# Kernel tuning notes

Hardware: AMD Instinct MI355X
Metric: run time of the kernel (lower is better)

Reference implementation:

```python
import jax, jax.numpy as jnp
import numpy as np

TIME_SCALES = [1, 2, 4]
K = len(TIME_SCALES)      # 3 scales
N = 4                     # lcm(time_scales)
S = sum(TIME_SCALES)      # 7 slots
D_HEAD = 128              # d
D = S * D_HEAD            # 896
IO_DIM = 1024
RANK = 64
HIDDEN = 4 * D            # 3584
EPS = 1e-5


def _tables():
    active = np.empty((N, K), dtype=np.int64)
    perm = np.empty((N, K, N), dtype=np.int64)
    inv = np.empty((N, K, N), dtype=np.int64)
    ids = np.arange(N)
    for ph in range(N):
        off = 0
        for k, s in enumerate(TIME_SCALES):
            active[ph, k] = off + ph % s
            off += s
            j = ph % s
            alpha = N // s
            p = (ids + alpha * j) % N   # SHARED assignment
            perm[ph, k] = p
            ip = np.empty_like(p)
            ip[p] = ids
            inv[ph, k] = ip
    return active, perm, inv

ACTIVE, PERM, INV = _tables()


def _ln(x, scale, bias):
    mu = jnp.mean(x, axis=-1, keepdims=True)
    var = jnp.mean((x - mu) ** 2, axis=-1, keepdims=True)
    return (x - mu) * jax.lax.rsqrt(var + EPS) * scale + bias


def setup_inputs() -> dict:
    key = jax.random.key(0)
    ks = jax.random.split(key, 16)
    B, T = 8, 1024

    def w(k, shape, s=0.02):
        return jax.random.normal(k, shape, dtype=jnp.float32) * s

    return {
        "x": jax.random.normal(ks[0], (B, T, IO_DIM), dtype=jnp.float32),
        "enc_base_w": w(ks[1], (D, IO_DIM)),
        "enc_A_w": w(ks[2], (RANK, IO_DIM)),
        "enc_B": w(ks[3], (RANK, N, D)),
        "enc_beta": jnp.float32(0.01),
        "Wqkv": w(ks[4], (K, N, D_HEAD, 3 * D_HEAD)),
        "ln_attn_scale": jnp.ones((D_HEAD,), jnp.float32),
        "ln_attn_bias": jnp.zeros((D_HEAD,), jnp.float32),
        "ln_mixer_scale": jnp.ones((D,), jnp.float32),
        "ln_mixer_bias": jnp.zeros((D,), jnp.float32),
        "mixer_w1": w(ks[5], (HIDDEN, D)),
        "mixer_b1": jnp.zeros((HIDDEN,), jnp.float32),
        "mixer_w2": w(ks[6], (D, HIDDEN)),
        "mixer_b2": jnp.zeros((D,), jnp.float32),
        "dec_ln_scale": jnp.ones((N * D,), jnp.float32),
        "dec_ln_bias": jnp.zeros((N * D,), jnp.float32),
        "dec_down_w": w(ks[7], (RANK, N * D)),
        "dec_up_w": w(ks[8], (IO_DIM, RANK)),
        "phase": 1,
    }


def reference(x, enc_base_w, enc_A_w, enc_B, enc_beta, Wqkv,
              ln_attn_scale, ln_attn_bias, ln_mixer_scale, ln_mixer_bias,
              mixer_w1, mixer_b1, mixer_w2, mixer_b2,
              dec_ln_scale, dec_ln_bias, dec_down_w, dec_up_w, phase):
    B, T, _ = x.shape
    # ---- StreamLoRAEncoder: x [B,T,io] -> z0 [B,T,N,D]
    base = x @ enc_base_w.T                 # [B,T,D]
    h = x @ enc_A_w.T                       # [B,T,r]
    delta = jnp.einsum('btr,rnd->btnd', h, enc_B)
    z0 = base[:, :, None, :] + enc_beta * delta
    # ---- gather active slots for this phase (one slot per scale group)
    slots = ACTIVE[phase]                   # [K]
    z_slots = z0.reshape(B, T, N, S, D_HEAD)
    x_slot = z_slots[:, :, :, slots, :]     # [B,T,N,K,d]
    x_slot = _ln(x_slot, ln_attn_scale, ln_attn_bias)
    # ---- SHARED qkv projection (stream->head inverse perm, bmm, head->stream perm)
    x_in = x_slot.transpose(0, 1, 3, 2, 4)  # [B,T,K,N,d]
    kk = np.arange(K)[:, None]
    x_head = x_in[:, :, kk, INV[phase], :]  # [B,T,K,N,d]
    qkv = jnp.einsum('btknd,knde->btkne', x_head, Wqkv)  # [B,T,K,N,3d]
    qh, kh, vh = jnp.split(qkv, 3, axis=-1)
    p = PERM[phase]
    q = qh[:, :, kk, p, :].transpose(0, 3, 2, 1, 4).reshape(B, N * K, T, D_HEAD)
    k_ = kh[:, :, kk, p, :].transpose(0, 3, 2, 1, 4).reshape(B, N * K, T, D_HEAD)
    v = vh[:, :, kk, p, :].transpose(0, 3, 2, 1, 4).reshape(B, N * K, T, D_HEAD)
    # ---- causal attention over T per (stream, scale) head
    scores = jnp.einsum('bhtd,bhsd->bhts', q, k_) / np.float32(np.sqrt(D_HEAD))
    mask = jnp.tril(jnp.ones((T, T), dtype=bool))
    scores = jnp.where(mask, scores, jnp.float32(-1e9))
    attn = jax.nn.softmax(scores, axis=-1)
    out = jnp.einsum('bhts,bhsd->bhtd', attn, v)  # [B,N*K,T,d]
    # ---- scatter back to active slots (residual add)
    out5 = out.reshape(B, N, K, T, D_HEAD).transpose(0, 3, 1, 2, 4)  # [B,T,N,K,d]
    z1 = z_slots.at[:, :, :, slots, :].add(out5).reshape(B, T, N, D)
    # ---- mixer MLP (pre-LN residual)
    hm = _ln(z1, ln_mixer_scale, ln_mixer_bias)
    m = jax.nn.gelu(hm @ mixer_w1.T + mixer_b1, approximate=False) @ mixer_w2.T + mixer_b2
    z2 = z1 + m
    # ---- StreamLoRADecoder: concat streams, LN, rank-bottleneck projection
    cat = z2.reshape(B, T, N * D)
    y = _ln(cat, dec_ln_scale, dec_ln_bias) @ dec_down_w.T @ dec_up_w.T
    return y
```

## Files before the change

kernel.cpp:

```cpp
#include <hip/hip_runtime.h>
#include <hip/hip_bf16.h>
#include <math.h>


#define BT   8192
#define DH   128
#define DD   896
#define ND   3584
#define IO   1024
#define RK   64
#define HID  3584

typedef __attribute__((ext_vector_type(8))) short short8;
typedef __attribute__((ext_vector_type(4))) float f32x4;
typedef __hip_bfloat16 bf16;

__device__ __forceinline__ float gelu_f(float v)
{
    float u = v * 0.70710678118654752f;
    float a = fabsf(u);
    float t = __builtin_amdgcn_rcpf(1.0f + 0.3275911f * a);
    float p = t * (0.254829592f + t * (-0.284496736f + t * (1.421413741f +
              t * (-1.453152027f + t * 1.061405429f))));
    float er = 1.0f - p * __expf(-u * u);
    er = copysignf(er, u);
    return 0.5f * v * (1.0f + er);
}

template<int BM, int BN, int BK, int TM, int TN>
__global__ __launch_bounds__(256) void gemm_kernel(const float* __restrict__ A,
                                                   const float* __restrict__ B,
                                                   float* __restrict__ C,
                                                   int N, int Kd)
{
    constexpr int THREADS = (BM / TM) * (BN / TN);
    constexpr int LDA = BM + 4;
    constexpr int LDB = BN + 4;
    __shared__ float As[BK][LDA];
    __shared__ float Bs[BK][LDB];

    const int tid = threadIdx.x;
    constexpr int NX = BN / TN;
    const int tx = tid % NX;
    const int ty = tid / NX;
    const int row0 = blockIdx.y * BM;
    const int col0 = blockIdx.x * BN;

    float acc[TM][TN];
#pragma unroll
    for (int i = 0; i < TM; ++i)
#pragma unroll
        for (int j = 0; j < TN; ++j) acc[i][j] = 0.f;

    for (int k0 = 0; k0 < Kd; k0 += BK) {
        constexpr int AF4 = BM * BK / 4;
        for (int f = tid; f < AF4; f += THREADS) {
            int r  = f / (BK / 4);
            int c4 = (f % (BK / 4)) * 4;
            float4 v = *(const float4*)(A + (size_t)(row0 + r) * Kd + k0 + c4);
            As[c4 + 0][r] = v.x; As[c4 + 1][r] = v.y;
            As[c4 + 2][r] = v.z; As[c4 + 3][r] = v.w;
        }
        constexpr int BF4 = BN * BK / 4;
        for (int f = tid; f < BF4; f += THREADS) {
            int r  = f / (BK / 4);
            int c4 = (f % (BK / 4)) * 4;
            float4 v = *(const float4*)(B + (size_t)(col0 + r) * Kd + k0 + c4);
            Bs[c4 + 0][r] = v.x; Bs[c4 + 1][r] = v.y;
            Bs[c4 + 2][r] = v.z; Bs[c4 + 3][r] = v.w;
        }
        __syncthreads();

#pragma unroll
        for (int kk = 0; kk < BK; ++kk) {
            float a[TM], b[TN];
#pragma unroll
            for (int i = 0; i < TM; i += 4)
                *(float4*)&a[i] = *(const float4*)&As[kk][ty * TM + i];
#pragma unroll
            for (int j = 0; j < TN; j += 4)
                *(float4*)&b[j] = *(const float4*)&Bs[kk][tx * TN + j];
#pragma unroll
            for (int i = 0; i < TM; ++i)
#pragma unroll
                for (int j = 0; j < TN; ++j)
                    acc[i][j] = fmaf(a[i], b[j], acc[i][j]);
        }
        __syncthreads();
    }

    const int crow = row0 + ty * TM;
    const int ccol = col0 + tx * TN;
#pragma unroll
    for (int i = 0; i < TM; ++i) {
        float* cp = C + (size_t)(crow + i) * N + ccol;
#pragma unroll
        for (int j = 0; j < TN; ++j) cp[j] = acc[i][j];
    }
}

template<int SPLIT>
__global__ __launch_bounds__(256) void gemm_splitk_kernel(const float* __restrict__ A,
                                                          const float* __restrict__ B,
                                                          float* __restrict__ C,
                                                          int N, int ld)
{
    __shared__ float As[16][68];
    __shared__ float Bs[16][68];
    const int tid = threadIdx.x;
    const int tx = tid & 15, ty = tid >> 4;
    const int row0 = blockIdx.y * 64;
    const int col0 = blockIdx.x * 64;
    const int kn   = ld / SPLIT;
    const int kbeg = blockIdx.z * kn;

    float acc[4][4];
#pragma unroll
    for (int i = 0; i < 4; ++i)
#pragma unroll
        for (int j = 0; j < 4; ++j) acc[i][j] = 0.f;

    for (int k0 = kbeg; k0 < kbeg + kn; k0 += 16) {
        {
            int r = tid >> 2, c4 = (tid & 3) << 2;
            float4 v = *(const float4*)(A + (size_t)(row0 + r) * ld + k0 + c4);
            As[c4 + 0][r] = v.x; As[c4 + 1][r] = v.y;
            As[c4 + 2][r] = v.z; As[c4 + 3][r] = v.w;
            float4 w = *(const float4*)(B + (size_t)(col0 + r) * ld + k0 + c4);
            Bs[c4 + 0][r] = w.x; Bs[c4 + 1][r] = w.y;
            Bs[c4 + 2][r] = w.z; Bs[c4 + 3][r] = w.w;
        }
        __syncthreads();
#pragma unroll
        for (int kk = 0; kk < 16; ++kk) {
            float a[4], b[4];
            *(float4*)a = *(const float4*)&As[kk][ty * 4];
            *(float4*)b = *(const float4*)&Bs[kk][tx * 4];
#pragma unroll
            for (int i = 0; i < 4; ++i)
#pragma unroll
                for (int j = 0; j < 4; ++j)
                    acc[i][j] = fmaf(a[i], b[j], acc[i][j]);
        }
        __syncthreads();
    }

#pragma unroll
    for (int i = 0; i < 4; ++i)
#pragma unroll
        for (int j = 0; j < 4; ++j)
            atomicAdd(C + (size_t)(row0 + ty * 4 + i) * N + col0 + tx * 4 + j,
                      acc[i][j]);
}

template<int EPI>
__global__ __launch_bounds__(256) void gemm_bf16_kernel(
    const bf16* __restrict__ A,
    const bf16* __restrict__ B,
    float* __restrict__ Cf,
    bf16* __restrict__ Cb,
    int N, int Kd,
    const float* __restrict__ bias)
{
    __shared__ bf16 As[128 * 64];
    __shared__ bf16 Bs[128 * 64];

    const int tid  = threadIdx.x;
    const int wave = tid >> 6;
    const int lane = tid & 63;
    const int wm = wave >> 1, wn = wave & 1;
    const int row0 = blockIdx.y * 128;
    const int col0 = blockIdx.x * 128;
    const int lr = lane & 15;
    const int lq = lane >> 4;
    const int srow = lane >> 3;
    const int scol = (lane & 7) * 8;

    f32x4 acc[4][4];
#pragma unroll
    for (int i = 0; i < 4; ++i)
#pragma unroll
        for (int j = 0; j < 4; ++j) acc[i][j] = (f32x4){0.f, 0.f, 0.f, 0.f};

    for (int k0 = 0; k0 < Kd; k0 += 64) {
#pragma unroll
        for (int j = 0; j < 4; ++j) {
            const int rg = wave * 32 + j * 8;
            __builtin_amdgcn_global_load_lds(
                (const __attribute__((address_space(1))) unsigned int*)
                    (A + (size_t)(row0 + rg + srow) * Kd + k0 + scol),
                (__attribute__((address_space(3))) unsigned int*)(As + rg * 64),
                16, 0, 0);
        }
#pragma unroll
        for (int j = 0; j < 4; ++j) {
            const int rg = wave * 32 + j * 8;
            __builtin_amdgcn_global_load_lds(
                (const __attribute__((address_space(1))) unsigned int*)
                    (B + (size_t)(col0 + rg + srow) * Kd + k0 + scol),
                (__attribute__((address_space(3))) unsigned int*)(Bs + rg * 64),
                16, 0, 0);
        }
        __syncthreads();

#pragma unroll
        for (int s = 0; s < 64; s += 32) {
            short8 af[4], bf[4];
#pragma unroll
            for (int mt = 0; mt < 4; ++mt)
                af[mt] = *(const short8*)&As[(wm * 64 + mt * 16 + lr) * 64 + s + lq * 8];
#pragma unroll
            for (int nt = 0; nt < 4; ++nt)
                bf[nt] = *(const short8*)&Bs[(wn * 64 + nt * 16 + lr) * 64 + s + lq * 8];
#pragma unroll
            for (int mt = 0; mt < 4; ++mt)
#pragma unroll
                for (int nt = 0; nt < 4; ++nt)
                    acc[mt][nt] = __builtin_amdgcn_mfma_f32_16x16x32_bf16(
                        af[mt], bf[nt], acc[mt][nt], 0, 0, 0);
        }
        __syncthreads();
    }

#pragma unroll
    for (int mt = 0; mt < 4; ++mt) {
#pragma unroll
        for (int nt = 0; nt < 4; ++nt) {
            const int col = col0 + wn * 64 + nt * 16 + lr;
            const float bcol = (EPI == 0) ? 0.f : bias[col];
#pragma unroll
            for (int r = 0; r < 4; ++r) {
                const int row = row0 + wm * 64 + mt * 16 + lq * 4 + r;
                float v = acc[mt][nt][r] + bcol;
                if (EPI == 1) {
                    Cb[(size_t)row * N + col] = __float2bfloat16(gelu_f(v));
                } else if (EPI == 2) {
                    Cf[(size_t)row * N + col] += v;
                } else {
                    Cf[(size_t)row * N + col] = v;
                }
            }
        }
    }
}

__global__ __launch_bounds__(256) void pack_enc_kernel(const float* __restrict__ baseW,
                                                       const float* __restrict__ Aw,
                                                       const float* __restrict__ Bv,
                                                       const float* __restrict__ betap,
                                                       bf16* __restrict__ outp)
{
    __shared__ float Ps[64][68];
    __shared__ float Qs[64][68];
    const int tid = threadIdx.x;
    const int e0 = blockIdx.y * 64;
    const int k0 = blockIdx.x * 64;

    for (int f = tid; f < 1024; f += 256) {
        int r = f >> 4, c4 = (f & 15) << 2;
        *(float4*)&Ps[r][c4] = *(const float4*)(Bv + (size_t)r * ND + e0 + c4);
        *(float4*)&Qs[r][c4] = *(const float4*)(Aw + (size_t)r * IO + k0 + c4);
    }
    __syncthreads();

    const int tx = tid & 15, ty = tid >> 4;
    float acc[4][4];
#pragma unroll
    for (int i = 0; i < 4; ++i)
#pragma unroll
        for (int j = 0; j < 4; ++j) acc[i][j] = 0.f;

#pragma unroll 8
    for (int r = 0; r < 64; ++r) {
        float a[4], b[4];
        *(float4*)a = *(const float4*)&Ps[r][ty * 4];
        *(float4*)b = *(const float4*)&Qs[r][tx * 4];
#pragma unroll
        for (int i = 0; i < 4; ++i)
#pragma unroll
            for (int j = 0; j < 4; ++j) acc[i][j] = fmaf(a[i], b[j], acc[i][j]);
    }

    const float beta = betap[0];
#pragma unroll
    for (int i = 0; i < 4; ++i) {
        const int e = e0 + ty * 4 + i;
        const int d = e % DD;
#pragma unroll
        for (int j = 0; j < 4; ++j) {
            const int k = k0 + tx * 4 + j;
            float v = baseW[(size_t)d * IO + k] + beta * acc[i][j];
            outp[(size_t)e * IO + k] = __float2bfloat16(v);
        }
    }
}

__global__ __launch_bounds__(256) void qkv_bf16_kernel(
    const bf16* __restrict__ xh,
    const bf16* __restrict__ Wt,
    bf16* __restrict__ Qg,
    bf16* __restrict__ Kg,
    bf16* __restrict__ Vtg,
    const int* __restrict__ phase_p,
    int go)
{
    __shared__ bf16 As[128 * 64];
    __shared__ bf16 Bs[128 * 64];

    const int ph  = phase_p[0] & 3;
    const int zbl = blockIdx.z;
    const int hh  = (go + zbl) % 12;
    const int n   = hh / 3;
    const int k   = hh % 3;
    const int m   = (k == 0) ? n
                  : (k == 1) ? ((n + 2 * (ph & 1)) & 3)
                             : ((n + (ph & 3)) & 3);
    const bf16* A  = xh + (size_t)zbl * (1024 * 128);
    const bf16* Bw = Wt + (size_t)(k * 4 + m) * (384 * 128);

    const int tid  = threadIdx.x;
    const int wave = tid >> 6;
    const int lane = tid & 63;
    const int wm = wave >> 1, wn = wave & 1;
    const int row0 = blockIdx.y * 128;
    const int col0 = blockIdx.x * 128;
    const int lr = lane & 15;
    const int lq = lane >> 4;
    const int srow = lane >> 3;
    const int scol = (lane & 7) * 8;

    f32x4 acc[4][4];
#pragma unroll
    for (int i = 0; i < 4; ++i)
#pragma unroll
        for (int j = 0; j < 4; ++j) acc[i][j] = (f32x4){0.f, 0.f, 0.f, 0.f};

#pragma unroll
    for (int k0 = 0; k0 < 128; k0 += 64) {
#pragma unroll
        for (int j = 0; j < 4; ++j) {
            const int rg = wave * 32 + j * 8;
            __builtin_amdgcn_global_load_lds(
                (const __attribute__((address_space(1))) unsigned int*)
                    (A + (size_t)(row0 + rg + srow) * 128 + k0 + scol),
                (__attribute__((address_space(3))) unsigned int*)(As + rg * 64),
                16, 0, 0);
        }
#pragma unroll
        for (int j = 0; j < 4; ++j) {
            const int rg = wave * 32 + j * 8;
            __builtin_amdgcn_global_load_lds(
                (const __attribute__((address_space(1))) unsigned int*)
                    (Bw + (size_t)(col0 + rg + srow) * 128 + k0 + scol),
                (__attribute__((address_space(3))) unsigned int*)(Bs + rg * 64),
                16, 0, 0);
        }
        __syncthreads();

#pragma unroll
        for (int s = 0; s < 64; s += 32) {
            short8 af[4], bf[4];
#pragma unroll
            for (int mt = 0; mt < 4; ++mt)
                af[mt] = *(const short8*)&As[(wm * 64 + mt * 16 + lr) * 64 + s + lq * 8];
#pragma unroll
            for (int nt = 0; nt < 4; ++nt)
                bf[nt] = *(const short8*)&Bs[(wn * 64 + nt * 16 + lr) * 64 + s + lq * 8];
#pragma unroll
            for (int mt = 0; mt < 4; ++mt)
#pragma unroll
                for (int nt = 0; nt < 4; ++nt)
                    acc[mt][nt] = __builtin_amdgcn_mfma_f32_16x16x32_bf16(
                        af[mt], bf[nt], acc[mt][nt], 0, 0, 0);
        }
        __syncthreads();
    }

    if (col0 < 256) {
        bf16* C = (col0 == 0 ? Qg : Kg) + (size_t)zbl * (1024 * 128);
#pragma unroll
        for (int mt = 0; mt < 4; ++mt)
#pragma unroll
            for (int nt = 0; nt < 4; ++nt) {
                const int col = wn * 64 + nt * 16 + lr;
#pragma unroll
                for (int r = 0; r < 4; ++r) {
                    const int row = row0 + wm * 64 + mt * 16 + lq * 4 + r;
                    C[(size_t)row * 128 + col] = __float2bfloat16(acc[mt][nt][r]);
                }
            }
    } else {
        bf16* Vt = Vtg + (size_t)zbl * (128 * 1024);
#pragma unroll
        for (int mt = 0; mt < 4; ++mt)
#pragma unroll
            for (int nt = 0; nt < 4; ++nt) {
                const int d = wn * 64 + nt * 16 + lr;
                const int rowb = row0 + wm * 64 + mt * 16 + lq * 4;
                union { bf16 h[4]; uint2 u; } pk;
#pragma unroll
                for (int r = 0; r < 4; ++r)
                    pk.h[r] = __float2bfloat16(acc[mt][nt][r]);
                *(uint2*)(Vt + (size_t)d * 1024 + rowb) = pk.u;
            }
    }
}

__global__ __launch_bounds__(256) void flash_bf16_kernel(
    const bf16* __restrict__ Qg,
    const bf16* __restrict__ Kg,
    const bf16* __restrict__ Vtg,
    float* __restrict__ z,
    const int* __restrict__ phase_p,
    int go)
{
    __shared__ bf16 Ks[64 * 128];
    __shared__ bf16 Vs[128 * 64];
    __shared__ bf16 Ps[64 * 64];

    const int ph  = phase_p[0] & 3;
    const int zbl = blockIdx.x;
    const int zb  = go + zbl;
    const int b   = zb / 12;
    const int hh  = zb % 12;
    const int n   = hh / 3;
    const int ks  = hh % 3;
    const int slot = (ks == 0) ? 0 : (ks == 1 ? 1 + (ph & 1) : 3 + (ph & 3));
    const int q0  = blockIdx.y * 64;

    const bf16* Qp = Qg  + (size_t)zbl * (1024 * 128);
    const bf16* Kp = Kg  + (size_t)zbl * (1024 * 128);
    const bf16* Vp = Vtg + (size_t)zbl * (128 * 1024);

    const int tid  = threadIdx.x;
    const int wave = tid >> 6;
    const int lane = tid & 63;
    const int lr = lane & 15;
    const int lq = lane >> 4;
    const int sr4 = lane >> 4, sc4 = (lane & 15) * 8;
    const int sr8 = lane >> 3, sc8 = (lane & 7) * 8;
    const int swz = (lr & 7) << 3;

    short8 qreg[4];
#pragma unroll
    for (int s = 0; s < 4; ++s)
        qreg[s] = *(const short8*)(Qp + (size_t)(q0 + wave * 16 + lr) * 128
                                   + s * 32 + lq * 8);

    f32x4 accO[8];
    float m_i[4], l_i[4];
#pragma unroll
    for (int j = 0; j < 8; ++j) accO[j] = (f32x4){0.f, 0.f, 0.f, 0.f};
#pragma unroll
    for (int r = 0; r < 4; ++r) { m_i[r] = -1e30f; l_i[r] = 0.f; }
    const float sc = 0.08838834764831845f;

    for (int j0 = 0; j0 <= q0; j0 += 64) {
#pragma unroll
        for (int j = 0; j < 4; ++j) {
            const int rg = wave * 16 + j * 4;
            const int krow = rg + sr4;
            const int kcol = sc4 ^ ((krow & 7) << 3);
            __builtin_amdgcn_global_load_lds(
                (const __attribute__((address_space(1))) unsigned int*)
                    (Kp + (size_t)(j0 + krow) * 128 + kcol),
                (__attribute__((address_space(3))) unsigned int*)(Ks + rg * 128),
                16, 0, 0);
        }
#pragma unroll
        for (int j = 0; j < 4; ++j) {
            const int rg = wave * 32 + j * 8;
            const int vrow = rg + sr8;
            const int vcol = sc8 ^ ((vrow & 7) << 3);
            __builtin_amdgcn_global_load_lds(
                (const __attribute__((address_space(1))) unsigned int*)
                    (Vp + (size_t)vrow * 1024 + j0 + vcol),
                (__attribute__((address_space(3))) unsigned int*)(Vs + rg * 64),
                16, 0, 0);
        }
        __syncthreads();

        f32x4 accS[4];
#pragma unroll
        for (int nt = 0; nt < 4; ++nt) accS[nt] = (f32x4){0.f, 0.f, 0.f, 0.f};
#pragma unroll
        for (int s = 0; s < 4; ++s) {
            short8 bk[4];
#pragma unroll
            for (int nt = 0; nt < 4; ++nt)
                bk[nt] = *(const short8*)&Ks[(nt * 16 + lr) * 128
                                             + ((s * 32 + lq * 8) ^ swz)];
#pragma unroll
            for (int nt = 0; nt < 4; ++nt)
                accS[nt] = __builtin_amdgcn_mfma_f32_16x16x32_bf16(
                    qreg[s], bk[nt], accS[nt], 0, 0, 0);
        }

        const bool need_mask = (j0 == q0);
#pragma unroll
        for (int r = 0; r < 4; ++r) {
            const int row = q0 + wave * 16 + lq * 4 + r;
            float sv[4];
#pragma unroll
            for (int nt = 0; nt < 4; ++nt) {
                float v = accS[nt][r] * sc;
                if (need_mask && (j0 + nt * 16 + lr > row)) v = -1e30f;
                sv[nt] = v;
            }
            float mx = fmaxf(fmaxf(sv[0], sv[1]), fmaxf(sv[2], sv[3]));
#pragma unroll
            for (int msk = 8; msk; msk >>= 1) mx = fmaxf(mx, __shfl_xor(mx, msk, 16));
            float mnew = fmaxf(m_i[r], mx);
            float al   = __expf(m_i[r] - mnew);
            float rs = 0.f;
#pragma unroll
            for (int nt = 0; nt < 4; ++nt) {
                sv[nt] = __expf(sv[nt] - mnew);
                rs += sv[nt];
            }
#pragma unroll
            for (int msk = 8; msk; msk >>= 1) rs += __shfl_xor(rs, msk, 16);
            l_i[r] = l_i[r] * al + rs;
            m_i[r] = mnew;
#pragma unroll
            for (int d8 = 0; d8 < 8; ++d8) accO[d8][r] *= al;
            const int prow = wave * 16 + lq * 4 + r;
            const int pswz = (prow & 7) << 3;
#pragma unroll
            for (int nt = 0; nt < 4; ++nt)
                Ps[prow * 64 + ((nt * 16 + lr) ^ pswz)] = __float2bfloat16(sv[nt]);
        }

#pragma unroll
        for (int kvs = 0; kvs < 64; kvs += 32) {
            short8 ap = *(const short8*)&Ps[(wave * 16 + lr) * 64
                                            + ((kvs + lq * 8) ^ swz)];
            short8 bv[8];
#pragma unroll
            for (int d8 = 0; d8 < 8; ++d8)
                bv[d8] = *(const short8*)&Vs[(d8 * 16 + lr) * 64
                                             + ((kvs + lq * 8) ^ swz)];
#pragma unroll
            for (int d8 = 0; d8 < 8; ++d8)
                accO[d8] = __builtin_amdgcn_mfma_f32_16x16x32_bf16(
                    ap, bv[d8], accO[d8], 0, 0, 0);
        }
        __syncthreads();
    }

#pragma unroll
    for (int r = 0; r < 4; ++r) {
        const int t = q0 + wave * 16 + lq * 4 + r;
        const float inv = 1.0f / l_i[r];
        float* dst = z + (size_t)(b * 1024 + t) * ND + n * DD + slot * DH;
#pragma unroll
        for (int d8 = 0; d8 < 8; ++d8)
            dst[d8 * 16 + lr] += accO[d8][r] * inv;
    }
}

__global__ __launch_bounds__(256) void cvt_bf16_kernel(const float* __restrict__ src,
                                                       bf16* __restrict__ dst,
                                                       int n4)
{
    int i = blockIdx.x * 256 + threadIdx.x;
    if (i < n4) {
        float4 v = ((const float4*)src)[i];
        bf16* d = dst + (size_t)i * 4;
        d[0] = __float2bfloat16(v.x);
        d[1] = __float2bfloat16(v.y);
        d[2] = __float2bfloat16(v.z);
        d[3] = __float2bfloat16(v.w);
    }
}

__global__ __launch_bounds__(256) void cvt_wqkv_kernel(const float* __restrict__ W,
                                                       bf16* __restrict__ Wt)
{
    int o = blockIdx.x * 256 + threadIdx.x;
    if (o < 12 * 384 * 128) {
        int i = o / 49152, rem = o % 49152;
        int e = rem / 128, d = rem % 128;
        Wt[o] = __float2bfloat16(W[(size_t)i * 49152 + d * 384 + e]);
    }
}

__global__ __launch_bounds__(256) void ln_attn_kernel(const float* __restrict__ z,
                                                      bf16* __restrict__ xh,
                                                      const float* __restrict__ scale,
                                                      const float* __restrict__ bias,
                                                      const int* __restrict__ phase_p,
                                                      int bt0)
{
    const int ph   = phase_p[0] & 3;
    const int lane = threadIdx.x & 63;
    const int row  = blockIdx.x * 4 + (threadIdx.x >> 6);
    const int k    = row % 3;
    const int n    = (row / 3) & 3;
    const int btl  = row / 12;
    const int slot = (k == 0) ? 0 : (k == 1 ? 1 + (ph & 1) : 3 + (ph & 3));
    const int bt   = bt0 + btl;

    const float* src = z + (size_t)bt * ND + n * DD + slot * DH + lane * 2;
    float2 v = *(const float2*)src;
    float s = v.x + v.y;
    float q = v.x * v.x + v.y * v.y;
#pragma unroll
    for (int m = 32; m; m >>= 1) { s += __shfl_xor(s, m); q += __shfl_xor(q, m); }
    float mu  = s * (1.0f / 128.0f);
    float var = q * (1.0f / 128.0f) - mu * mu;
    float r   = rsqrtf(var + 1e-5f);

    float2 sc2 = *(const float2*)(scale + lane * 2);
    float2 bi2 = *(const float2*)(bias + lane * 2);
    const int bl = btl >> 10, t = btl & 1023;
    union { bf16 h[2]; unsigned int u; } pk;
    pk.h[0] = __float2bfloat16((v.x - mu) * r * sc2.x + bi2.x);
    pk.h[1] = __float2bfloat16((v.y - mu) * r * sc2.y + bi2.y);
    *(unsigned int*)(xh + (size_t)((bl * 12 + n * 3 + k) * 1024 + t) * DH + lane * 2) = pk.u;
}

template<int W>
__global__ __launch_bounds__(256) void ln_row_kernel(const float* __restrict__ in,
                                                     float* __restrict__ outp,
                                                     const float* __restrict__ scale,
                                                     const float* __restrict__ bias)
{
    constexpr int NIT = (W + 255) / 256;
    const int row = blockIdx.x;
    const int tid = threadIdx.x;
    const float* rp = in + (size_t)row * W;

    float v[NIT];
    float s = 0.f, q = 0.f;
#pragma unroll
    for (int i = 0; i < NIT; ++i) {
        int idx = tid + i * 256;
        if (idx < W) { float t = rp[idx]; v[i] = t; s += t; q += t * t; }
        else v[i] = 0.f;
    }
#pragma unroll
    for (int m = 32; m; m >>= 1) { s += __shfl_xor(s, m); q += __shfl_xor(q, m); }
    __shared__ float ss[4], sq[4];
    if ((tid & 63) == 0) { ss[tid >> 6] = s; sq[tid >> 6] = q; }
    __syncthreads();
    s = ss[0] + ss[1] + ss[2] + ss[3];
    q = sq[0] + sq[1] + sq[2] + sq[3];
    float mu  = s * (1.0f / W);
    float var = q * (1.0f / W) - mu * mu;
    float r   = rsqrtf(var + 1e-5f);

    float* op = outp + (size_t)row * W;
#pragma unroll
    for (int i = 0; i < NIT; ++i) {
        int idx = tid + i * 256;
        if (idx < W) op[idx] = (v[i] - mu) * r * scale[idx] + bias[idx];
    }
}

__global__ __launch_bounds__(256) void ln_row_bf16_kernel(const float* __restrict__ in,
                                                          bf16* __restrict__ outp,
                                                          const float* __restrict__ scale,
                                                          const float* __restrict__ bias)
{
    constexpr int W = 896, NIT = 4;
    const int row = blockIdx.x;
    const int tid = threadIdx.x;
    const float* rp = in + (size_t)row * W;

    float v[NIT];
    float s = 0.f, q = 0.f;
#pragma unroll
    for (int i = 0; i < NIT; ++i) {
        int idx = tid + i * 256;
        if (idx < W) { float t = rp[idx]; v[i] = t; s += t; q += t * t; }
        else v[i] = 0.f;
    }
#pragma unroll
    for (int m = 32; m; m >>= 1) { s += __shfl_xor(s, m); q += __shfl_xor(q, m); }
    __shared__ float ss[4], sq[4];
    if ((tid & 63) == 0) { ss[tid >> 6] = s; sq[tid >> 6] = q; }
    __syncthreads();
    s = ss[0] + ss[1] + ss[2] + ss[3];
    q = sq[0] + sq[1] + sq[2] + sq[3];
    float mu  = s * (1.0f / W);
    float var = q * (1.0f / W) - mu * mu;
    float r   = rsqrtf(var + 1e-5f);

    bf16* op = outp + (size_t)row * W;
#pragma unroll
    for (int i = 0; i < NIT; ++i) {
        int idx = tid + i * 256;
        if (idx < W)
            op[idx] = __float2bfloat16((v[i] - mu) * r * scale[idx] + bias[idx]);
    }
}

extern "C" void kernel_launch(void* const* d_in, const int* in_sizes, int n_in,
                              void* d_out, int out_size, void* d_ws, size_t ws_size,
                              hipStream_t stream)
{
    const float* x          = (const float*)d_in[0];
    const float* enc_base_w = (const float*)d_in[1];
    const float* enc_A_w    = (const float*)d_in[2];
    const float* enc_B      = (const float*)d_in[3];
    const float* enc_beta   = (const float*)d_in[4];
    const float* Wqkv       = (const float*)d_in[5];
    const float* ln_attn_s  = (const float*)d_in[6];
    const float* ln_attn_b  = (const float*)d_in[7];
    const float* ln_mix_s   = (const float*)d_in[8];
    const float* ln_mix_b   = (const float*)d_in[9];
    const float* w1         = (const float*)d_in[10];
    const float* b1         = (const float*)d_in[11];
    const float* w2         = (const float*)d_in[12];
    const float* b2         = (const float*)d_in[13];
    const float* dec_ln_s   = (const float*)d_in[14];
    const float* dec_ln_b   = (const float*)d_in[15];
    const float* dec_down   = (const float*)d_in[16];
    const float* dec_up     = (const float*)d_in[17];
    const int*   phase_p    = (const int*)d_in[18];
    float* out = (float*)d_out;

    float* ws = (float*)d_ws;
    float* z  = ws;
    float* R  = ws + (size_t)BT * ND;

    const int GQ = (ws_size >= 230000000UL) ? 96 : 48;
    const int CH = (ws_size >= 205000000UL) ? 8192 : 4096;

    bf16* xb   = (bf16*)R;
    bf16* Wenc = xb + (size_t)BT * IO;
    bf16* Wt   = (bf16*)R;
    bf16* xh_b = Wt + 12 * 384 * 128;
    bf16* Qb   = xh_b + (size_t)GQ * 1024 * 128;
    bf16* Kb   = Qb + (size_t)GQ * 1024 * 128;
    bf16* Vtg  = Kb + (size_t)GQ * 1024 * 128;
    bf16* w1b  = (bf16*)R;
    bf16* w2b  = w1b + (size_t)HID * DD;
    bf16* hm   = w2b + (size_t)DD * HID;
    bf16* gbuf = hm + (size_t)CH * DD;
    float* t1  = R;

    cvt_bf16_kernel<<<dim3(8192), 256, 0, stream>>>(x, xb, BT * IO / 4);
    pack_enc_kernel<<<dim3(16, 56), 256, 0, stream>>>(enc_base_w, enc_A_w, enc_B,
                                                      enc_beta, Wenc);
    gemm_bf16_kernel<0><<<dim3(28, 64), 256, 0, stream>>>(xb, Wenc, z, nullptr,
                                                          ND, IO, nullptr);

    cvt_wqkv_kernel<<<dim3(2304), 256, 0, stream>>>(Wqkv, Wt);
    const int ngroups = 96 / GQ;
    for (int g = 0; g < ngroups; ++g) {
        ln_attn_kernel<<<dim3(GQ * 256), 256, 0, stream>>>(z, xh_b, ln_attn_s,
                                                           ln_attn_b, phase_p,
                                                           g * (GQ / 12) * 1024);
        qkv_bf16_kernel<<<dim3(3, 8, GQ), 256, 0, stream>>>(xh_b, Wt, Qb, Kb, Vtg,
                                                            phase_p, g * GQ);
        flash_bf16_kernel<<<dim3(GQ, 16), 256, 0, stream>>>(Qb, Kb, Vtg, z,
                                                            phase_p, g * GQ);
    }

    cvt_bf16_kernel<<<dim3(3136), 256, 0, stream>>>(w1, w1b, HID * DD / 4);
    cvt_bf16_kernel<<<dim3(3136), 256, 0, stream>>>(w2, w2b, DD * HID / 4);
    for (int c = 0; c < 32768 / CH; ++c) {
        float* zc = z + (size_t)c * CH * DD;
        ln_row_bf16_kernel<<<dim3(CH), 256, 0, stream>>>(zc, hm, ln_mix_s, ln_mix_b);
        gemm_bf16_kernel<1><<<dim3(28, CH / 128), 256, 0, stream>>>(
            hm, w1b, nullptr, gbuf, HID, DD, b1);
        gemm_bf16_kernel<2><<<dim3(7, CH / 128), 256, 0, stream>>>(
            gbuf, w2b, zc, nullptr, DD, HID, b2);
    }

    ln_row_kernel<3584><<<dim3(8192), 256, 0, stream>>>(z, z, dec_ln_s, dec_ln_b);
    hipMemsetAsync(t1, 0, (size_t)BT * RK * sizeof(float), stream);
    gemm_splitk_kernel<8><<<dim3(1, 128, 8), 256, 0, stream>>>(z, dec_down, t1,
                                                               RK, ND);
    gemm_kernel<128, 128, 16, 8, 8>
        <<<dim3(8, 64), 256, 0, stream>>>(t1, dec_up, out, IO, RK);
}
```

Baseline: 1.399 ms.

## Replace bf16 GEMM with 256-row tiled, 4-stage pipelined, swizzled-LDS kernel

Replaces the 128x128 bf16 MFMA GEMM with a 512-thread kernel using 256xBN tiles. It keeps a 4-slot ring of asynchronous global-to-LDS loads with explicit vmcnt waits, so loads overlap MFMA work instead of syncing every K step. It also XOR-swizzles the LDS layout to reduce bank conflicts, remaps block IDs across 8 groups for cache locality, and raises wave priority around MFMA bursts. The larger tiles and 8xNR accumulators raise register and LDS pressure. The hand-written waitcnt counts are tied to the load counts per stage.

After: 1.360 ms. 1.03x faster.

```diff
diff --git a/kernel.cpp b/kernel.cpp
--- a/kernel.cpp
+++ b/kernel.cpp
@@ -153,8 +153,8 @@
                       acc[i][j]);
 }
 
-template<int EPI>
-__global__ __launch_bounds__(256) void gemm_bf16_kernel(
+template<int BN, int EPI>
+__global__ __launch_bounds__(512, 2) void gemm_bf16_256(
     const bf16* __restrict__ A,
     const bf16* __restrict__ B,
     float* __restrict__ Cf,
@@ -162,75 +162,132 @@
     int N, int Kd,
     const float* __restrict__ bias)
 {
-    __shared__ bf16 As[128 * 64];
-    __shared__ bf16 Bs[128 * 64];
+    constexpr int NR    = BN / 64;
+    constexpr int WTN   = 16 * NR;
+    constexpr int ASLOT = 256 * 32;
+    constexpr int BSLOT = BN * 32;
+    __shared__ bf16 As[4 * ASLOT];
+    __shared__ bf16 Bs[4 * BSLOT];
 
     const int tid  = threadIdx.x;
     const int wave = tid >> 6;
     const int lane = tid & 63;
-    const int wm = wave >> 1, wn = wave & 1;
-    const int row0 = blockIdx.y * 128;
-    const int col0 = blockIdx.x * 128;
-    const int lr = lane & 15;
-    const int lq = lane >> 4;
-    const int srow = lane >> 3;
-    const int scol = (lane & 7) * 8;
-
-    f32x4 acc[4][4];
-#pragma unroll
-    for (int i = 0; i < 4; ++i)
-#pragma unroll
-        for (int j = 0; j < 4; ++j) acc[i][j] = (f32x4){0.f, 0.f, 0.f, 0.f};
-
-    for (int k0 = 0; k0 < Kd; k0 += 64) {
-#pragma unroll
-        for (int j = 0; j < 4; ++j) {
-            const int rg = wave * 32 + j * 8;
+    const int wm = wave >> 2, wn = wave & 3;
+    const int lr = lane & 15, lq = lane >> 4;
+
+    const int gx  = gridDim.x;
+    int fid = blockIdx.y * gx + blockIdx.x;
+    const int cpx = (gx * gridDim.y) >> 3;
+    fid = (fid & 7) * cpx + (fid >> 3);
+    const int row0 = (fid / gx) * 256;
+    const int col0 = (fid % gx) * BN;
+
+    const int sr  = lane >> 2;
+    const int scs = (((lane & 3) ^ ((lane >> 3) & 3)) << 3);
+    const bf16* Ag = A + (size_t)(row0 + sr) * Kd + scs;
+    const bf16* Bg = B + (size_t)(col0 + sr) * Kd + scs;
+
+    const int scox = (lq * 8) ^ (((lr >> 1) & 3) << 3);
+
+    f32x4 acc[8][NR];
+#pragma unroll
+    for (int i = 0; i < 8; ++i)
+#pragma unroll
+        for (int j = 0; j < NR; ++j) acc[i][j] = (f32x4){0.f, 0.f, 0.f, 0.f};
+
+    const int NH = Kd >> 5;
+
+    auto stage = [&](int h) {
+        const int slot = h & 3;
+#pragma unroll
+        for (int i = 0; i < 2; ++i) {
+            const int rg = (i * 8 + wave) * 16;
             __builtin_amdgcn_global_load_lds(
                 (const __attribute__((address_space(1))) unsigned int*)
-                    (A + (size_t)(row0 + rg + srow) * Kd + k0 + scol),
-                (__attribute__((address_space(3))) unsigned int*)(As + rg * 64),
+                    (Ag + (size_t)rg * Kd + h * 32),
+                (__attribute__((address_space(3))) unsigned int*)
+                    (As + slot * ASLOT + rg * 32),
                 16, 0, 0);
         }
 #pragma unroll
-        for (int j = 0; j < 4; ++j) {
-            const int rg = wave * 32 + j * 8;
+        for (int i = 0; i < BN / 128; ++i) {
+            const int rg = (i * 8 + wave) * 16;
             __builtin_amdgcn_global_load_lds(
                 (const __attribute__((address_space(1))) unsigned int*)
-                    (B + (size_t)(col0 + rg + srow) * Kd + k0 + scol),
-                (__attribute__((address_space(3))) unsigned int*)(Bs + rg * 64),
+                    (Bg + (size_t)rg * Kd + h * 32),
+                (__attribute__((address_space(3))) unsigned int*)
+                    (Bs + slot * BSLOT + rg * 32),
                 16, 0, 0);
         }
-        __syncthreads();
-
-#pragma unroll
-        for (int s = 0; s < 64; s += 32) {
-            short8 af[4], bf[4];
-#pragma unroll
-            for (int mt = 0; mt < 4; ++mt)
-                af[mt] = *(const short8*)&As[(wm * 64 + mt * 16 + lr) * 64 + s + lq * 8];
-#pragma unroll
-            for (int nt = 0; nt < 4; ++nt)
-                bf[nt] = *(const short8*)&Bs[(wn * 64 + nt * 16 + lr) * 64 + s + lq * 8];
-#pragma unroll
-            for (int mt = 0; mt < 4; ++mt)
-#pragma unroll
-                for (int nt = 0; nt < 4; ++nt)
-                    acc[mt][nt] = __builtin_amdgcn_mfma_f32_16x16x32_bf16(
-                        af[mt], bf[nt], acc[mt][nt], 0, 0, 0);
-        }
-        __syncthreads();
-    }
-
-#pragma unroll
-    for (int mt = 0; mt < 4; ++mt) {
-#pragma unroll
-        for (int nt = 0; nt < 4; ++nt) {
-            const int col = col0 + wn * 64 + nt * 16 + lr;
+    };
+
+    stage(0); stage(1); stage(2);
+
+    for (int h = 0; h < NH; ++h) {
+        if (h + 3 < NH) stage(h + 3);
+
+        const int ahead = NH - 1 - h;
+        if constexpr (BN == 256) {
+            if (ahead >= 3)      asm volatile("s_waitcnt vmcnt(12)" ::: "memory");
+            else if (ahead == 2) asm volatile("s_waitcnt vmcnt(8)"  ::: "memory");
+            else if (ahead == 1) asm volatile("s_waitcnt vmcnt(4)"  ::: "memory");
+            else                 asm volatile("s_waitcnt vmcnt(0)"  ::: "memory");
+        } else {
+            if (ahead >= 3)      asm volatile("s_waitcnt vmcnt(9)"  ::: "memory");
+            else if (ahead == 2) asm volatile("s_waitcnt vmcnt(6)"  ::: "memory");
+            else if (ahead == 1) asm volatile("s_waitcnt vmcnt(3)"  ::: "memory");
+            else                 asm volatile("s_waitcnt vmcnt(0)"  ::: "memory");
+        }
+        __builtin_amdgcn_s_barrier();
+        __builtin_amdgcn_sched_barrier(0);
+
+        const bf16* Ab = As + (h & 3) * ASLOT;
+        const bf16* Bb = Bs + (h & 3) * BSLOT;
+
+        short8 bfr[NR], af[4], af2[4];
+#pragma unroll
+        for (int nt = 0; nt < NR; ++nt)
+            bfr[nt] = *(const short8*)&Bb[(wn * WTN + nt * 16 + lr) * 32 + scox];
+#pragma unroll
+        for (int mt = 0; mt < 4; ++mt)
+            af[mt] = *(const short8*)&Ab[(wm * 128 + mt * 16 + lr) * 32 + scox];
+
+        __builtin_amdgcn_s_setprio(1);
+#pragma unroll
+        for (int mt = 0; mt < 4; ++mt)
+#pragma unroll
+            for (int nt = 0; nt < NR; ++nt)
+                acc[mt][nt] = __builtin_amdgcn_mfma_f32_16x16x32_bf16(
+                    af[mt], bfr[nt], acc[mt][nt], 0, 0, 0);
+        __builtin_amdgcn_s_setprio(0);
+
+#pragma unroll
+        for (int mt = 0; mt < 4; ++mt)
+            af2[mt] = *(const short8*)&Ab[(wm * 128 + 64 + mt * 16 + lr) * 32 + scox];
+
+        __builtin_amdgcn_s_setprio(1);
+#pragma unroll
+        for (int mt = 0; mt < 4; ++mt)
+#pragma unroll
+            for (int nt = 0; nt < NR; ++nt)
+                acc[mt + 4][nt] = __builtin_amdgcn_mfma_f32_16x16x32_bf16(
+                    af2[mt], bfr[nt], acc[mt + 4][nt], 0, 0, 0);
+        __builtin_amdgcn_s_setprio(0);
+
+        asm volatile("s_waitcnt lgkmcnt(0)" ::: "memory");
+        __builtin_amdgcn_sched_barrier(0);
+        __builtin_amdgcn_s_barrier();
+    }
+
+#pragma unroll
+    for (int mt = 0; mt < 8; ++mt) {
+#pragma unroll
+        for (int nt = 0; nt < NR; ++nt) {
+            const int col = col0 + wn * WTN + nt * 16 + lr;
             const float bcol = (EPI == 0) ? 0.f : bias[col];
 #pragma unroll
             for (int r = 0; r < 4; ++r) {
-                const int row = row0 + wm * 64 + mt * 16 + lq * 4 + r;
+                const int row = row0 + wm * 128 + mt * 16 + lq * 4 + r;
                 float v = acc[mt][nt][r] + bcol;
                 if (EPI == 1) {
                     Cb[(size_t)row * N + col] = __float2bfloat16(gelu_f(v));
@@ -744,8 +801,8 @@
     cvt_bf16_kernel<<<dim3(8192), 256, 0, stream>>>(x, xb, BT * IO / 4);
     pack_enc_kernel<<<dim3(16, 56), 256, 0, stream>>>(enc_base_w, enc_A_w, enc_B,
                                                       enc_beta, Wenc);
-    gemm_bf16_kernel<0><<<dim3(28, 64), 256, 0, stream>>>(xb, Wenc, z, nullptr,
-                                                          ND, IO, nullptr);
+    gemm_bf16_256<256, 0><<<dim3(14, 32), 512, 0, stream>>>(xb, Wenc, z, nullptr,
+                                                            ND, IO, nullptr);
 
     cvt_wqkv_kernel<<<dim3(2304), 256, 0, stream>>>(Wqkv, Wt);
     const int ngroups = 96 / GQ;
@@ -764,9 +821,9 @@
     for (int c = 0; c < 32768 / CH; ++c) {
         float* zc = z + (size_t)c * CH * DD;
         ln_row_bf16_kernel<<<dim3(CH), 256, 0, stream>>>(zc, hm, ln_mix_s, ln_mix_b);
-        gemm_bf16_kernel<1><<<dim3(28, CH / 128), 256, 0, stream>>>(
+        gemm_bf16_256<256, 1><<<dim3(14, CH / 256), 512, 0, stream>>>(
             hm, w1b, nullptr, gbuf, HID, DD, b1);
-        gemm_bf16_kernel<2><<<dim3(7, CH / 128), 256, 0, stream>>>(
+        gemm_bf16_256<128, 2><<<dim3(7, CH / 256), 512, 0, stream>>>(
             gbuf, w2b, zc, nullptr, DD, HID, b2);
     }
 
```
